# Kernel tuning notes

Hardware: AMD Instinct MI355X
Metric: run time of the kernel (lower is better)

Reference implementation:

```python
import jax, jax.numpy as jnp
import numpy as np


def _mlp2(x, w1, b1, w2, b2):
    # 2-layer MLP with exact GELU (matches torch nn.GELU default)
    h = jax.nn.gelu(x @ w1 + b1, approximate=False)
    return h @ w2 + b2


def setup_inputs() -> dict:
    B, nx = 16, 16384
    d_latent, d_hidden, k = 64, 128, 3
    key = jax.random.key(0)
    ks = jax.random.split(key, 14)
    s = 0.1
    inp = {
        "u0": jax.random.normal(ks[0], (B, nx), dtype=jnp.float32),
        "x": jax.random.uniform(ks[1], (B, nx), dtype=jnp.float32),
        # node_mlp: 2 -> d_hidden -> d_latent
        "node_w1": jax.random.normal(ks[2], (2, d_hidden), dtype=jnp.float32) * s,
        "node_b1": jnp.zeros((d_hidden,), dtype=jnp.float32),
        "node_w2": jax.random.normal(ks[3], (d_hidden, d_latent), dtype=jnp.float32) * s,
        "node_b2": jnp.zeros((d_latent,), dtype=jnp.float32),
        # edge_mlp: 3 -> d_hidden -> d_latent
        "edge_w1": jax.random.normal(ks[4], (3, d_hidden), dtype=jnp.float32) * s,
        "edge_b1": jnp.zeros((d_hidden,), dtype=jnp.float32),
        "edge_w2": jax.random.normal(ks[5], (d_hidden, d_latent), dtype=jnp.float32) * s,
        "edge_b2": jnp.zeros((d_latent,), dtype=jnp.float32),
        # combine: 2*d_latent -> d_hidden -> d_latent
        "comb_w1": jax.random.normal(ks[6], (2 * d_latent, d_hidden), dtype=jnp.float32) * s,
        "comb_b1": jnp.zeros((d_hidden,), dtype=jnp.float32),
        "comb_w2": jax.random.normal(ks[7], (d_hidden, d_latent), dtype=jnp.float32) * s,
        "comb_b2": jnp.zeros((d_latent,), dtype=jnp.float32),
        "k": k,
    }
    return inp


def reference(u0, x, node_w1, node_b1, node_w2, node_b2,
              edge_w1, edge_b1, edge_w2, edge_b2,
              comb_w1, comb_b1, comb_w2, comb_b2, k):
    B, nx = u0.shape
    # h_self = node_mlp([u_i, x_i])                       -> [B, nx, d_latent]
    h_self = _mlp2(jnp.stack([u0, x], axis=-1), node_w1, node_b1, node_w2, node_b2)

    # Replicate-padded neighbor gather == clamp indices to [0, nx-1]
    offs = jnp.arange(-k, k + 1)                          # [2k+1]
    idx = jnp.clip(jnp.arange(nx)[None, :] + offs[:, None], 0, nx - 1)  # [2k+1, nx]
    u_j = u0[:, idx]                                      # [B, 2k+1, nx]
    dx = x[:, idx] - x[:, None, :]                        # [B, 2k+1, nx]
    u_i = jnp.broadcast_to(u0[:, None, :], u_j.shape)

    # edge_mlp over all neighbors at once, then sum over neighbor axis
    edge_in = jnp.stack([u_i, u_j, dx], axis=-1)          # [B, 2k+1, nx, 3]
    agg = _mlp2(edge_in, edge_w1, edge_b1, edge_w2, edge_b2).sum(axis=1)  # [B, nx, d_latent]

    return _mlp2(jnp.concatenate([h_self, agg], axis=-1), comb_w1, comb_b1, comb_w2, comb_b2)
```

## Files before the change

kernel.cpp:

```cpp
#include <hip/hip_runtime.h>
#include <hip/hip_bf16.h>

#define NXc 16384
#define DHc 128
#define DLc 64
#define Kc  3
#define Wc  7
#define Pc  32
#define NTc 256
#define HALO 38
#define RB  272
#define RBc 272

typedef __attribute__((ext_vector_type(8))) short short8;
typedef __attribute__((ext_vector_type(4))) float f32x4;

#define OFF_U  0
#define OFF_X  160
#define OFF_C  320
#define OFF_HC OFF_C
#define OFF_GN 10656
#define OFF_H2 OFF_GN
#define OFF_S  19360
#define SMEM_BYTES 28064

#define WS_NW2 0
#define WS_EW2 8192
#define WS_CW1 16384
#define WS_CW2 32768
#define WS_TOTAL 40960

#if __has_builtin(__builtin_amdgcn_exp2f)
#define EXP2F(x) __builtin_amdgcn_exp2f(x)
#else
#define EXP2F(x) exp2f(x)
#endif
#if __has_builtin(__builtin_amdgcn_rcpf)
#define RCPF(x) __builtin_amdgcn_rcpf(x)
#else
#define RCPF(x) (1.0f / (x))
#endif

#define GC0 -2.30220838f
#define GC1 -0.10294325f

__device__ __forceinline__ void gelu2(float x0, float x1, float& g0, float& g1) {
    x0 = fmaxf(x0, -8.0f);
    x1 = fmaxf(x1, -8.0f);
    float e0 = EXP2F(x0 * fmaf(GC1, x0 * x0, GC0));
    float e1 = EXP2F(x1 * fmaf(GC1, x1 * x1, GC0));
    float t0 = 1.0f + e0, t1 = 1.0f + e1;
    float rr = RCPF(t0 * t1);
    g0 = x0 * t1 * rr;
    g1 = x1 * t0 * rr;
}

__device__ __forceinline__ void gelu2_acc(float x0, float x1, float& a0, float& a1) {
    float e0 = EXP2F(x0 * fmaf(GC1, x0 * x0, GC0));
    float e1 = EXP2F(x1 * fmaf(GC1, x1 * x1, GC0));
    float t0 = 1.0f + e0, t1 = 1.0f + e1;
    float rr = RCPF(t0 * t1);
    a0 = fmaf(x0 * t1, rr, a0);
    a1 = fmaf(x1 * t0, rr, a1);
}

__device__ __forceinline__ unsigned bf16rne(float a) {
    unsigned u;
    __builtin_memcpy(&u, &a, 4);
    return u + 0x7FFFu + ((u >> 16) & 1u);
}
__device__ __forceinline__ unsigned pack_bf16(float a, float b) {
    return (bf16rne(a) >> 16) | (bf16rne(b) & 0xFFFF0000u);
}
__device__ __forceinline__ void store_bf16x4(void* p, float a, float b, float c, float d) {
    uint2 u;
    u.x = pack_bf16(a, b);
    u.y = pack_bf16(c, d);
    *(uint2*)p = u;
}
__device__ __forceinline__ float bf_lo(unsigned u) {
    unsigned v = u << 16;
    float f; __builtin_memcpy(&f, &v, 4);
    return f;
}
__device__ __forceinline__ float bf_hi(unsigned u) {
    unsigned v = u & 0xFFFF0000u;
    float f; __builtin_memcpy(&f, &v, 4);
    return f;
}

__global__ void pack_weights(const float* __restrict__ nw2, const float* __restrict__ ew2,
                             const float* __restrict__ cw1, const float* __restrict__ cw2,
                             __hip_bfloat16* __restrict__ ws)
{
    int idx = blockIdx.x * 256 + threadIdx.x;
    const float* src;
    int N, base, e;
    if (idx < 8192)       { src = nw2; N = 64;  base = WS_NW2; e = idx; }
    else if (idx < 16384) { src = ew2; N = 64;  base = WS_EW2; e = idx - 8192; }
    else if (idx < 32768) { src = cw1; N = 128; base = WS_CW1; e = idx - 16384; }
    else                  { src = cw2; N = 64;  base = WS_CW2; e = idx - 32768; }
    int f = e >> 9, l = (e >> 3) & 63, j = e & 7;
    int nt = f >> 2, kt = f & 3;
    int k = kt * 32 + (l >> 4) * 8 + j;
    int n = nt * 16 + (l & 15);
    ws[base + e] = __float2bfloat16(src[k * N + n]);
}

__global__ __launch_bounds__(NTc, 5)
void lifting_mfma(const float* __restrict__ u0, const float* __restrict__ x,
                  const float* __restrict__ nw1, const float* __restrict__ nb1,
                  const float* __restrict__ nb2, const float* __restrict__ eb1,
                  const float* __restrict__ eb2, const float* __restrict__ cb1,
                  const float* __restrict__ cb2, const float* __restrict__ ew1,
                  const short8* __restrict__ wsv, float* __restrict__ out)
{
    __shared__ char sm[SMEM_BYTES];
    float* s_u = (float*)(sm + OFF_U);
    float* s_x = (float*)(sm + OFF_X);

    const int tid   = threadIdx.x;
    const int wave  = tid >> 6;
    const int lane  = tid & 63;
    const int quad  = lane >> 4;
    const int l15   = lane & 15;
    const int tiles = NXc / Pc;
    const int b     = blockIdx.x / tiles;
    const int i0    = (blockIdx.x % tiles) * Pc;
    const float* ub = u0 + (size_t)b * NXc;
    const float* xb = x  + (size_t)b * NXc;

    if (tid < HALO) {
        int i = i0 - Kc + tid;
        i = i < 0 ? 0 : (i >= NXc ? NXc - 1 : i);
        s_u[tid] = ub[i];
        s_x[tid] = xb[i];
    }
    __syncthreads();

    {
        const int j2 = tid & 63;
        const int r0 = tid >> 6;
        const int j  = j2 * 2;
        float2 wa = *(const float2*)(ew1 + DHc + j);
        float2 wb = *(const float2*)(ew1 + 2 * DHc + j);
        for (int t = r0; t < HALO; t += 4) {
            float uu = s_u[t], xx = s_x[t];
            float c0 = fmaf(uu, wa.x, xx * wb.x);
            float c1 = fmaf(uu, wa.y, xx * wb.y);
            *(unsigned*)(sm + OFF_C + t * RBc + j2 * 4) = pack_bf16(c0, c1);
        }
    }
    __syncthreads();

    {
        const int jq = tid & 31, pbase = tid >> 5;
        const int j0 = jq * 4;
        const float4 w0 = *(const float4*)(nw1 + j0);
        const float4 w1 = *(const float4*)(nw1 + DHc + j0);
        const float4 nb = *(const float4*)(nb1 + j0);
        const float4 e0 = *(const float4*)(ew1 + j0);
        const float4 e2 = *(const float4*)(ew1 + 2 * DHc + j0);
        const float4 be = *(const float4*)(eb1 + j0);
        #pragma unroll
        for (int r = 0; r < 4; ++r) {
            const int p = pbase + 8 * r;
            const float uu = s_u[p + Kc], xx = s_x[p + Kc];

            float g0, g1, g2, g3;
            gelu2(fmaf(uu, w0.x, fmaf(xx, w1.x, nb.x)),
                  fmaf(uu, w0.y, fmaf(xx, w1.y, nb.y)), g0, g1);
            gelu2(fmaf(uu, w0.z, fmaf(xx, w1.z, nb.z)),
                  fmaf(uu, w0.w, fmaf(xx, w1.w, nb.w)), g2, g3);
            store_bf16x4(sm + OFF_GN + p * RB + j0 * 2, g0, g1, g2, g3);

            float a0 = fmaf(uu, e0.x, -(xx * e2.x)) + be.x;
            float a1 = fmaf(uu, e0.y, -(xx * e2.y)) + be.y;
            float a2 = fmaf(uu, e0.z, -(xx * e2.z)) + be.z;
            float a3 = fmaf(uu, e0.w, -(xx * e2.w)) + be.w;
            float acc0 = 0.f, acc1 = 0.f, acc2 = 0.f, acc3 = 0.f;
            const char* crow = sm + OFF_C + p * RBc + jq * 8;
            #pragma unroll
            for (int o = 0; o < Wc; ++o) {
                uint2 cp = *(const uint2*)(crow + o * RBc);
                gelu2_acc(a0 + bf_lo(cp.x), a1 + bf_hi(cp.x), acc0, acc1);
                gelu2_acc(a2 + bf_lo(cp.y), a3 + bf_hi(cp.y), acc2, acc3);
            }
            store_bf16x4(sm + OFF_S + p * RB + j0 * 2, acc0, acc1, acc2, acc3);
        }
    }
    __syncthreads();

    {
        const int mt = wave & 1, mat = wave >> 1;
        const int rowbase = mt * 16;
        const int aoff = mat ? OFF_S : OFF_GN;
        const short8* Bmat = wsv + (mat ? (WS_EW2 >> 3) : (WS_NW2 >> 3));
        f32x4 acc[4] = {{0,0,0,0},{0,0,0,0},{0,0,0,0},{0,0,0,0}};
        #pragma unroll
        for (int kt = 0; kt < 4; ++kt) {
            short8 af = *(const short8*)(sm + aoff + (rowbase + l15) * RB + kt * 64 + quad * 16);
            #pragma unroll
            for (int nt = 0; nt < 4; ++nt) {
                short8 wf = Bmat[(nt * 4 + kt) * 64 + lane];
                acc[nt] = __builtin_amdgcn_mfma_f32_16x16x32_bf16(wf, af, acc[nt], 0, 0, 0);
            }
        }
        const float* bias = mat ? eb2 : nb2;
        const float bscale = mat ? 7.f : 1.f;
        const int colhalf = mat ? DLc : 0;
        const int p = rowbase + l15;
        #pragma unroll
        for (int nt = 0; nt < 4; ++nt) {
            float4 bv = ((const float4*)bias)[nt * 4 + quad];
            store_bf16x4(sm + OFF_HC + p * RB + (colhalf + nt * 16 + quad * 4) * 2,
                         fmaf(bscale, bv.x, acc[nt][0]),
                         fmaf(bscale, bv.y, acc[nt][1]),
                         fmaf(bscale, bv.z, acc[nt][2]),
                         fmaf(bscale, bv.w, acc[nt][3]));
        }
    }
    __syncthreads();

    {
        const int mt = wave & 1, nh = wave >> 1;
        const int rowbase = mt * 16;
        const short8* Bmat = wsv + (WS_CW1 >> 3);
        f32x4 acc[4] = {{0,0,0,0},{0,0,0,0},{0,0,0,0},{0,0,0,0}};
        #pragma unroll
        for (int kt = 0; kt < 4; ++kt) {
            short8 af = *(const short8*)(sm + OFF_HC + (rowbase + l15) * RB + kt * 64 + quad * 16);
            #pragma unroll
            for (int t = 0; t < 4; ++t) {
                int nt = nh * 4 + t;
                short8 wf = Bmat[(nt * 4 + kt) * 64 + lane];
                acc[t] = __builtin_amdgcn_mfma_f32_16x16x32_bf16(wf, af, acc[t], 0, 0, 0);
            }
        }
        const int p = rowbase + l15;
        #pragma unroll
        for (int t = 0; t < 4; ++t) {
            int nbase = (nh * 4 + t) * 16 + quad * 4;
            float4 cb = ((const float4*)cb1)[nbase >> 2];
            float h0, h1, h2v, h3;
            gelu2(acc[t][0] + cb.x, acc[t][1] + cb.y, h0, h1);
            gelu2(acc[t][2] + cb.z, acc[t][3] + cb.w, h2v, h3);
            store_bf16x4(sm + OFF_H2 + p * RB + nbase * 2, h0, h1, h2v, h3);
        }
    }
    __syncthreads();

    {
        const int mt = wave & 1, nh = wave >> 1;
        const int rowbase = mt * 16;
        const short8* Bmat = wsv + (WS_CW2 >> 3);
        f32x4 acc[2] = {{0,0,0,0},{0,0,0,0}};
        #pragma unroll
        for (int kt = 0; kt < 4; ++kt) {
            short8 af = *(const short8*)(sm + OFF_H2 + (rowbase + l15) * RB + kt * 64 + quad * 16);
            #pragma unroll
            for (int t = 0; t < 2; ++t) {
                int nt = nh * 2 + t;
                short8 wf = Bmat[(nt * 4 + kt) * 64 + lane];
                acc[t] = __builtin_amdgcn_mfma_f32_16x16x32_bf16(wf, af, acc[t], 0, 0, 0);
            }
        }
        const int p = rowbase + l15;
        float* outb = out + ((size_t)b * NXc + i0 + p) * DLc;
        #pragma unroll
        for (int t = 0; t < 2; ++t) {
            int nbase = (nh * 2 + t) * 16 + quad * 4;
            float4 cb = ((const float4*)cb2)[nbase >> 2];
            float4 v;
            v.x = acc[t][0] + cb.x;
            v.y = acc[t][1] + cb.y;
            v.z = acc[t][2] + cb.z;
            v.w = acc[t][3] + cb.w;
            *(float4*)(outb + nbase) = v;
        }
    }
}

extern "C" void kernel_launch(void* const* d_in, const int* in_sizes, int n_in,
                              void* d_out, int out_size, void* d_ws, size_t ws_size,
                              hipStream_t stream) {
    const float* u0  = (const float*)d_in[0];
    const float* x   = (const float*)d_in[1];
    const float* nw1 = (const float*)d_in[2];
    const float* nb1 = (const float*)d_in[3];
    const float* nw2 = (const float*)d_in[4];
    const float* nb2 = (const float*)d_in[5];
    const float* ew1 = (const float*)d_in[6];
    const float* eb1 = (const float*)d_in[7];
    const float* ew2 = (const float*)d_in[8];
    const float* eb2 = (const float*)d_in[9];
    const float* cw1 = (const float*)d_in[10];
    const float* cb1 = (const float*)d_in[11];
    const float* cw2 = (const float*)d_in[12];
    const float* cb2 = (const float*)d_in[13];
    float* out = (float*)d_out;

    __hip_bfloat16* ws = (__hip_bfloat16*)d_ws;
    pack_weights<<<WS_TOTAL / 256, 256, 0, stream>>>(nw2, ew2, cw1, cw2, ws);

    const int grid = 16 * (NXc / Pc);
    lifting_mfma<<<grid, NTc, 0, stream>>>(u0, x, nw1, nb1, nb2, eb1, eb2, cb1, cb2,
                                           ew1, (const short8*)d_ws, out);
}
```

Before: 202.8 us.

## Compute neighbor edge terms in registers instead of a shared-memory bf16 table

Drops the shared-memory stage that precomputed per-halo-point edge first-layer contributions as bf16, along with one barrier. Each thread now handles 4 consecutive points and computes the 10 needed neighbor terms in fp32 registers, reusing them across the sliding window. Shared memory shrinks, the occupancy hint rises from 5 to 6, and bf16 packing uses a hardware pack instruction when available. The cost is higher register pressure from the cw[10][4] array, which may conflict with the higher occupancy target.

After: 198.6 us. 1.02x faster.

```diff
diff --git a/kernel.cpp b/kernel.cpp
--- a/kernel.cpp
+++ b/kernel.cpp
@@ -10,19 +10,17 @@
 #define NTc 256
 #define HALO 38
 #define RB  272
-#define RBc 272
 
 typedef __attribute__((ext_vector_type(8))) short short8;
 typedef __attribute__((ext_vector_type(4))) float f32x4;
 
 #define OFF_U  0
 #define OFF_X  160
-#define OFF_C  320
-#define OFF_HC OFF_C
-#define OFF_GN 10656
+#define OFF_GN 320
 #define OFF_H2 OFF_GN
-#define OFF_S  19360
-#define SMEM_BYTES 28064
+#define OFF_S  9024
+#define OFF_HC 17728
+#define SMEM_BYTES 26432
 
 #define WS_NW2 0
 #define WS_EW2 8192
@@ -64,6 +62,13 @@
     a1 = fmaf(x1 * t0, rr, a1);
 }
 
+#if __has_builtin(__builtin_amdgcn_cvt_pk_bf16_f32)
+typedef __attribute__((ext_vector_type(2))) __bf16 bf16x2_t;
+__device__ __forceinline__ unsigned pack_bf16(float a, float b) {
+    bf16x2_t v = __builtin_amdgcn_cvt_pk_bf16_f32(a, b);
+    unsigned r; __builtin_memcpy(&r, &v, 4); return r;
+}
+#else
 __device__ __forceinline__ unsigned bf16rne(float a) {
     unsigned u;
     __builtin_memcpy(&u, &a, 4);
@@ -72,21 +77,12 @@
 __device__ __forceinline__ unsigned pack_bf16(float a, float b) {
     return (bf16rne(a) >> 16) | (bf16rne(b) & 0xFFFF0000u);
 }
+#endif
 __device__ __forceinline__ void store_bf16x4(void* p, float a, float b, float c, float d) {
     uint2 u;
     u.x = pack_bf16(a, b);
     u.y = pack_bf16(c, d);
     *(uint2*)p = u;
-}
-__device__ __forceinline__ float bf_lo(unsigned u) {
-    unsigned v = u << 16;
-    float f; __builtin_memcpy(&f, &v, 4);
-    return f;
-}
-__device__ __forceinline__ float bf_hi(unsigned u) {
-    unsigned v = u & 0xFFFF0000u;
-    float f; __builtin_memcpy(&f, &v, 4);
-    return f;
 }
 
 __global__ void pack_weights(const float* __restrict__ nw2, const float* __restrict__ ew2,
@@ -107,7 +103,7 @@
     ws[base + e] = __float2bfloat16(src[k * N + n]);
 }
 
-__global__ __launch_bounds__(NTc, 5)
+__global__ __launch_bounds__(NTc, 6)
 void lifting_mfma(const float* __restrict__ u0, const float* __restrict__ x,
                   const float* __restrict__ nw1, const float* __restrict__ nb1,
                   const float* __restrict__ nb2, const float* __restrict__ eb1,
@@ -139,33 +135,37 @@
     __syncthreads();
 
     {
-        const int j2 = tid & 63;
-        const int r0 = tid >> 6;
-        const int j  = j2 * 2;
-        float2 wa = *(const float2*)(ew1 + DHc + j);
-        float2 wb = *(const float2*)(ew1 + 2 * DHc + j);
-        for (int t = r0; t < HALO; t += 4) {
-            float uu = s_u[t], xx = s_x[t];
-            float c0 = fmaf(uu, wa.x, xx * wb.x);
-            float c1 = fmaf(uu, wa.y, xx * wb.y);
-            *(unsigned*)(sm + OFF_C + t * RBc + j2 * 4) = pack_bf16(c0, c1);
-        }
-    }
-    __syncthreads();
-
-    {
-        const int jq = tid & 31, pbase = tid >> 5;
+        const int jq = tid & 31;
+        const int pbase = (tid >> 5) * 4;
         const int j0 = jq * 4;
         const float4 w0 = *(const float4*)(nw1 + j0);
         const float4 w1 = *(const float4*)(nw1 + DHc + j0);
         const float4 nb = *(const float4*)(nb1 + j0);
         const float4 e0 = *(const float4*)(ew1 + j0);
+        const float4 e1 = *(const float4*)(ew1 + DHc + j0);
         const float4 e2 = *(const float4*)(ew1 + 2 * DHc + j0);
         const float4 be = *(const float4*)(eb1 + j0);
-        #pragma unroll
-        for (int r = 0; r < 4; ++r) {
-            const int p = pbase + 8 * r;
-            const float uu = s_u[p + Kc], xx = s_x[p + Kc];
+
+        float su[10], sx[10];
+        #pragma unroll
+        for (int r = 0; r < 10; ++r) {
+            su[r] = s_u[pbase + r];
+            sx[r] = s_x[pbase + r];
+        }
+
+        float cw[10][4];
+        #pragma unroll
+        for (int r = 0; r < 10; ++r) {
+            cw[r][0] = fmaf(su[r], e1.x, sx[r] * e2.x);
+            cw[r][1] = fmaf(su[r], e1.y, sx[r] * e2.y);
+            cw[r][2] = fmaf(su[r], e1.z, sx[r] * e2.z);
+            cw[r][3] = fmaf(su[r], e1.w, sx[r] * e2.w);
+        }
+
+        #pragma unroll
+        for (int r0 = 0; r0 < 4; ++r0) {
+            const int p = pbase + r0;
+            const float uu = su[r0 + 3], xx = sx[r0 + 3];
 
             float g0, g1, g2, g3;
             gelu2(fmaf(uu, w0.x, fmaf(xx, w1.x, nb.x)),
@@ -179,12 +179,11 @@
             float a2 = fmaf(uu, e0.z, -(xx * e2.z)) + be.z;
             float a3 = fmaf(uu, e0.w, -(xx * e2.w)) + be.w;
             float acc0 = 0.f, acc1 = 0.f, acc2 = 0.f, acc3 = 0.f;
-            const char* crow = sm + OFF_C + p * RBc + jq * 8;
             #pragma unroll
             for (int o = 0; o < Wc; ++o) {
-                uint2 cp = *(const uint2*)(crow + o * RBc);
-                gelu2_acc(a0 + bf_lo(cp.x), a1 + bf_hi(cp.x), acc0, acc1);
-                gelu2_acc(a2 + bf_lo(cp.y), a3 + bf_hi(cp.y), acc2, acc3);
+                const float* cr = cw[r0 + o];
+                gelu2_acc(a0 + cr[0], a1 + cr[1], acc0, acc1);
+                gelu2_acc(a2 + cr[2], a3 + cr[3], acc2, acc3);
             }
             store_bf16x4(sm + OFF_S + p * RB + j0 * 2, acc0, acc1, acc2, acc3);
         }
```
